# Optimization experiments

Measured on AMD Instinct MI355X. Metric: run time of the kernel, lower is better.

The kernel has to match this reference:

```python
import jax, jax.numpy as jnp
import numpy as np

NS_STEPS = 10
NS_A, NS_B, NS_C = 3.4445, -4.7750, 2.0315  # standard quintic Newton-Schulz coefficients
EPS = 1e-7

def orthogonalize(w):
    """Newton-Schulz iteration producing a (near-)orthogonal matrix from w."""
    din, dout = w.shape
    transpose = din > dout  # iterate on the wide orientation so X @ X.T is small
    x = w.T if transpose else w
    x = x / (jnp.linalg.norm(x) + EPS)  # spectral norm <= frobenius norm -> contraction

    def body(x, _):
        a = x @ x.T                      # (m, m) Gram matrix
        bmat = NS_B * a + NS_C * (a @ a)
        x = NS_A * x + bmat @ x
        return x, None

    x, _ = jax.lax.scan(body, x, None, length=NS_STEPS)
    return x.T if transpose else x


def setup_inputs() -> dict:
    key = jax.random.key(0)
    k1, k2, k3 = jax.random.split(key, 3)
    B, DIN, DOUT = 16384, 2048, 2048
    x = jax.random.normal(k1, (B, DIN), dtype=jnp.float32)
    w = jax.random.normal(k2, (DIN, DOUT), dtype=jnp.float32)
    b = jax.random.normal(k3, (DOUT,), dtype=jnp.float32) * 0.02
    return {"x": x, "w": w, "b": b}


def reference(x, w, b):
    w_orth = orthogonalize(w)
    return x @ w_orth + b
```

## Files before the change

kernel.cpp:

```cpp
#include <hip/hip_runtime.h>
#include <stdint.h>

typedef unsigned short u16;
typedef _Float16 half_t;
typedef __attribute__((ext_vector_type(4))) float f32x4;
typedef __attribute__((ext_vector_type(8))) _Float16 f16x8;

#define NS_A 3.4445f
#define NS_B -4.7750f
#define NS_C 2.0315f

#define SX      64.0f
#define INV_SX  (1.0f / 64.0f)
#define INV_SA  (1.0f / 4096.0f)

typedef const __attribute__((address_space(1))) void* as1_cvp;
typedef __attribute__((address_space(3))) void* as3_vp;
#define GLOAD_LDS16(gp, lp) \
    __builtin_amdgcn_global_load_lds((as1_cvp)(const void*)(gp), (as3_vp)(void*)(lp), 16, 0, 0)

template <int N> __device__ __forceinline__ void vmwait() {
    if constexpr (N == 0)       asm volatile("s_waitcnt vmcnt(0)" ::: "memory");
    else if constexpr (N == 4)  asm volatile("s_waitcnt vmcnt(4)" ::: "memory");
    else if constexpr (N == 6)  asm volatile("s_waitcnt vmcnt(6)" ::: "memory");
    else if constexpr (N == 8)  asm volatile("s_waitcnt vmcnt(8)" ::: "memory");
    else if constexpr (N == 12) asm volatile("s_waitcnt vmcnt(12)" ::: "memory");
    else static_assert(N == 0, "unsupported vmcnt");
}

template <int MODE>
__global__ __launch_bounds__(256, 2) void gemm_ns(
    const half_t* __restrict__ A, const half_t* __restrict__ B,
    const half_t* __restrict__ aux,
    void* __restrict__ outp, half_t* __restrict__ outpT,
    int M, int N, int K)
{
    __shared__ half_t As[3][64 * 64];
    __shared__ half_t Bs[3][128 * 64];
    const int tid  = threadIdx.x;
    const int wid  = tid >> 6;
    const int lane = tid & 63;
    const int wr = wid >> 1, wc = wid & 1;

    const int xcd = blockIdx.x & 7;
    const int ii  = blockIdx.x >> 3;
    const int brow = ((xcd & 1) * 16 + (ii >> 2)) * 64;
    const int bcol = ((xcd >> 1) * 4 + (ii & 3)) * 128;

    f32x4 acc[2][4] = {};

    const int r0   = tid >> 3;
    const int csrc = ((tid & 7) ^ ((tid >> 3) & 7)) * 8;
    const half_t* gA = A + (size_t)(brow + r0) * K + csrc;
    const half_t* gB = B + (size_t)(bcol + r0) * K + csrc;

    auto stage = [&](int slot, int kt) {
#pragma unroll
        for (int j = 0; j < 2; ++j)
            GLOAD_LDS16(gA + (size_t)(j * 32) * K + kt, &As[slot][(j * 256 + wid * 64) * 8]);
#pragma unroll
        for (int j = 0; j < 4; ++j)
            GLOAD_LDS16(gB + (size_t)(j * 32) * K + kt, &Bs[slot][(j * 256 + wid * 64) * 8]);
    };

    f16x8 af[2][2], bf[4][2];
    auto reads = [&](int slot) {
#pragma unroll
        for (int m = 0; m < 2; ++m) {
            const int row = wr * 32 + m * 16 + (lane & 15);
#pragma unroll
            for (int kk = 0; kk < 2; ++kk) {
                const int cc = (kk * 4 + (lane >> 4)) ^ (row & 7);
                af[m][kk] = *(const f16x8*)&As[slot][row * 64 + cc * 8];
            }
        }
#pragma unroll
        for (int n = 0; n < 4; ++n) {
            const int row = wc * 64 + n * 16 + (lane & 15);
#pragma unroll
            for (int kk = 0; kk < 2; ++kk) {
                const int cc = (kk * 4 + (lane >> 4)) ^ (row & 7);
                bf[n][kk] = *(const f16x8*)&Bs[slot][row * 64 + cc * 8];
            }
        }
    };
    auto mfma = [&]() {
        __builtin_amdgcn_s_setprio(1);
#pragma unroll
        for (int kk = 0; kk < 2; ++kk)
#pragma unroll
            for (int m = 0; m < 2; ++m)
#pragma unroll
                for (int n = 0; n < 4; ++n)
                    acc[m][n] = __builtin_amdgcn_mfma_f32_16x16x32_f16(af[m][kk], bf[n][kk], acc[m][n], 0, 0, 0);
        __builtin_amdgcn_s_setprio(0);
    };

    const int nsteps = K / 64;
    stage(0, 0);
    stage(1, 64);
    vmwait<6>();
    __builtin_amdgcn_s_barrier();

    int s = 0;
    for (; s < nsteps - 2; ++s) {
        reads(s % 3);
        stage((s + 2) % 3, (s + 2) * 64);
        vmwait<6>();
        __builtin_amdgcn_s_barrier();
        mfma();
        __builtin_amdgcn_s_barrier();
    }
    reads(s % 3);
    vmwait<0>();
    __builtin_amdgcn_s_barrier();
    mfma();
    __builtin_amdgcn_s_barrier();
    ++s;
    reads(s % 3);
    mfma();

#pragma unroll
    for (int m = 0; m < 2; ++m) {
#pragma unroll
        for (int n = 0; n < 4; ++n) {
            const int row0 = brow + wr * 32 + m * 16 + (lane >> 4) * 4;
            const int col  = bcol + wc * 64 + n * 16 + (lane & 15);
#pragma unroll
            for (int r = 0; r < 4; ++r) {
                const size_t idx = (size_t)(row0 + r) * N + col;
                const float v = acc[m][n][r];
                if (MODE == 0) {
                    ((half_t*)outp)[idx] = (half_t)v;
                } else if (MODE == 1) {
                    ((half_t*)outp)[idx] = (half_t)(NS_B * (float)aux[idx] + NS_C * v * INV_SA);
                } else {
                    const half_t o = (half_t)(NS_A * (float)aux[idx] + v * INV_SA);
                    ((half_t*)outp)[idx] = o;
                    if (outpT) outpT[(size_t)col * M + row0 + r] = o;
                }
            }
        }
    }
}

__global__ __launch_bounds__(512) void gemm_fin(
    const half_t* __restrict__ A, const half_t* __restrict__ B,
    const float* __restrict__ bias, float* __restrict__ out,
    int M, int N, int K)
{
    __shared__ half_t As[2][256 * 32];
    __shared__ half_t Bs[2][256 * 32];
    const int tid  = threadIdx.x;
    const int wid  = tid >> 6;
    const int lane = tid & 63;
    const int wm = wid >> 2;
    const int wn = wid & 3;

    int bid = blockIdx.x;
    const int cpx = gridDim.x >> 3;
    bid = (bid & 7) * cpx + (bid >> 3);
    const int nbx  = N >> 8;
    const int brow = (bid / nbx) << 8;
    const int bcol = (bid % nbx) << 8;

    f32x4 acc[8][4] = {};

    const int r0   = tid >> 2;
    const int csrc = ((tid & 3) ^ ((tid >> 3) & 3)) * 8;
    const half_t* gA = A + (size_t)(brow + r0) * K + csrc;
    const half_t* gB = B + (size_t)(bcol + r0) * K + csrc;

    auto stage = [&](int slot, int kt) {
#pragma unroll
        for (int j = 0; j < 2; ++j)
            GLOAD_LDS16(gA + (size_t)(j * 128) * K + kt, &As[slot][(j * 512 + wid * 64) * 8]);
#pragma unroll
        for (int j = 0; j < 2; ++j)
            GLOAD_LDS16(gB + (size_t)(j * 128) * K + kt, &Bs[slot][(j * 512 + wid * 64) * 8]);
    };
    auto compute = [&](int slot) {
        f16x8 af[8], bf[4];
#pragma unroll
        for (int fr = 0; fr < 8; ++fr) {
            const int row = wm * 128 + fr * 16 + (lane & 15);
            af[fr] = *(const f16x8*)&As[slot][row * 32 + (((lane >> 4) ^ ((row >> 1) & 3)) * 8)];
        }
#pragma unroll
        for (int fc = 0; fc < 4; ++fc) {
            const int row = wn * 64 + fc * 16 + (lane & 15);
            bf[fc] = *(const f16x8*)&Bs[slot][row * 32 + (((lane >> 4) ^ ((row >> 1) & 3)) * 8)];
        }
        __builtin_amdgcn_s_setprio(1);
#pragma unroll
        for (int fr = 0; fr < 8; ++fr)
#pragma unroll
            for (int fc = 0; fc < 4; ++fc)
                acc[fr][fc] = __builtin_amdgcn_mfma_f32_16x16x32_f16(af[fr], bf[fc], acc[fr][fc], 0, 0, 0);
        __builtin_amdgcn_s_setprio(0);
    };

    const int nsteps = K >> 5;
    stage(0, 0);
    vmwait<0>();
    __builtin_amdgcn_s_barrier();

    for (int s = 0; s < nsteps; ++s) {
        const int slot = s & 1;
        if (s + 1 < nsteps) stage(slot ^ 1, (s + 1) * 32);
        compute(slot);
        if (s + 1 < nsteps) {
            vmwait<0>();
            __builtin_amdgcn_s_barrier();
        }
    }

#pragma unroll
    for (int fr = 0; fr < 8; ++fr) {
#pragma unroll
        for (int fc = 0; fc < 4; ++fc) {
            const int row0 = brow + wm * 128 + fr * 16 + (lane >> 4) * 4;
            const int col  = bcol + wn * 64 + fc * 16 + (lane & 15);
            const float bv = bias[col];
#pragma unroll
            for (int r = 0; r < 4; ++r)
                out[(size_t)(row0 + r) * N + col] = acc[fr][fc][r] * INV_SX + bv;
        }
    }
}

__global__ __launch_bounds__(256) void k_sumsq(const float* __restrict__ w,
                                               float* __restrict__ part, int n) {
    __shared__ float s[256];
    const int per  = n / 1024;
    const int base = blockIdx.x * per;
    float acc = 0.f;
    for (int i = threadIdx.x; i < per; i += 256) {
        float v = w[base + i];
        acc += v * v;
    }
    s[threadIdx.x] = acc;
    __syncthreads();
    for (int k = 128; k > 0; k >>= 1) {
        if (threadIdx.x < k) s[threadIdx.x] += s[threadIdx.x + k];
        __syncthreads();
    }
    if (threadIdx.x == 0) part[blockIdx.x] = s[0];
}

__global__ __launch_bounds__(256) void k_scalefin(const float* __restrict__ part,
                                                  float* __restrict__ scale) {
    __shared__ float s[256];
    float acc = 0.f;
    for (int i = threadIdx.x; i < 1024; i += 256) acc += part[i];
    s[threadIdx.x] = acc;
    __syncthreads();
    for (int k = 128; k > 0; k >>= 1) {
        if (threadIdx.x < k) s[threadIdx.x] += s[threadIdx.x + k];
        __syncthreads();
    }
    if (threadIdx.x == 0) scale[0] = SX / (sqrtf(s[0]) + 1e-7f);
}

__global__ __launch_bounds__(256) void k_scale_f16(const float* __restrict__ w,
                                                   const float* __restrict__ scale,
                                                   half_t* __restrict__ o, int n) {
    const int i = (blockIdx.x * 256 + threadIdx.x) * 4;
    if (i < n) {
        const float sc = scale[0];
        float4 v = *(const float4*)(w + i);
        o[i + 0] = (half_t)(v.x * sc);
        o[i + 1] = (half_t)(v.y * sc);
        o[i + 2] = (half_t)(v.z * sc);
        o[i + 3] = (half_t)(v.w * sc);
    }
}

__global__ __launch_bounds__(256) void k_cast_f16(const float* __restrict__ w,
                                                  half_t* __restrict__ o, int n) {
    const int i = (blockIdx.x * 256 + threadIdx.x) * 4;
    if (i < n) {
        float4 v = *(const float4*)(w + i);
        o[i + 0] = (half_t)v.x;
        o[i + 1] = (half_t)v.y;
        o[i + 2] = (half_t)v.z;
        o[i + 3] = (half_t)v.w;
    }
}

__global__ __launch_bounds__(256) void k_transpose(const u16* __restrict__ in,
                                                   u16* __restrict__ out, int n) {
    __shared__ u16 tile[64][65];
    const int bx = blockIdx.x * 64, by = blockIdx.y * 64;
    const int tx = threadIdx.x & 63, ty = threadIdx.x >> 6;
    for (int i = ty; i < 64; i += 4) tile[i][tx] = in[(size_t)(by + i) * n + bx + tx];
    __syncthreads();
    for (int i = ty; i < 64; i += 4) out[(size_t)(bx + i) * n + by + tx] = tile[tx][i];
}

extern "C" void kernel_launch(void* const* d_in, const int* in_sizes, int n_in,
                              void* d_out, int out_size, void* d_ws, size_t ws_size,
                              hipStream_t stream) {
    const float* x = (const float*)d_in[0];
    const float* w = (const float*)d_in[1];
    const float* b = (const float*)d_in[2];
    float* out = (float*)d_out;

    const int D  = 2048;
    const int Bm = in_sizes[0] / D;
    const int WN = D * D;
    const int XN = Bm * D;

    const size_t matB = (size_t)WN * 2;
    const bool pingpong = ws_size >= 8192 + 6 * matB + (size_t)XN * 2;

    char* ws = (char*)d_ws;
    float* part  = (float*)ws;
    float* scale = part + 1024;
    half_t* xb0  = (half_t*)(ws + 8192);
    half_t* xb1  = xb0 + WN;
    half_t* xbTa = xb1 + WN;
    half_t* xbTb = pingpong ? (xbTa + WN) : xbTa;
    half_t* amat = xbTb + WN;
    half_t* bmat = amat + WN;
    half_t* xinb = bmat + WN;

    k_sumsq<<<1024, 256, 0, stream>>>(w, part, WN);
    k_scalefin<<<1, 256, 0, stream>>>(part, scale);
    k_scale_f16<<<WN / 4 / 256, 256, 0, stream>>>(w, scale, xb0, WN);

    k_cast_f16<<<XN / 4 / 256, 256, 0, stream>>>(x, xinb, XN);

    const dim3 tgrid(D / 64, D / 64);
    k_transpose<<<tgrid, 256, 0, stream>>>((const u16*)xb0, (u16*)xbTa, D);

    const int ns_grid = (D / 64) * (D / 128);

    half_t* cur = xb0;
    half_t* nxt = xb1;
    half_t* Tr  = xbTa;
    half_t* Tw  = xbTb;
    for (int it = 0; it < 10; ++it) {
        gemm_ns<0><<<ns_grid, 256, 0, stream>>>(cur, cur, nullptr, amat, nullptr, D, D, D);
        gemm_ns<1><<<ns_grid, 256, 0, stream>>>(amat, amat, amat, bmat, nullptr, D, D, D);
        if (pingpong) {
            gemm_ns<2><<<ns_grid, 256, 0, stream>>>(bmat, Tr, cur, nxt, Tw, D, D, D);
            half_t* tt = Tr; Tr = Tw; Tw = tt;
        } else {
            gemm_ns<2><<<ns_grid, 256, 0, stream>>>(bmat, Tr, cur, nxt, nullptr, D, D, D);
            k_transpose<<<tgrid, 256, 0, stream>>>((const u16*)nxt, (u16*)Tr, D);
        }
        half_t* t = cur; cur = nxt; nxt = t;
    }

    const int fin_grid = (Bm / 256) * (D / 256);
    gemm_fin<<<fin_grid, 512, 0, stream>>>(xinb, Tr, b, out, Bm, D, D);
}
```

Before: 964.4 us.

## Deepen final GEMM K-tile, fuse scale with transpose, skip unused last store

The final x@W GEMM now stages 64-wide K tiles instead of 32, with an 8-way XOR swizzle, so it needs half as many barrier/wait steps per block, at the cost of doubled LDS use. The scale-to-f16 kernel is merged with the initial transpose, which removes one launch and one pass over the weight matrix. The last Newton-Schulz iteration skips writing the row-major output, since only the transposed copy is consumed afterwards.

```diff
diff --git a/kernel.cpp b/kernel.cpp
--- a/kernel.cpp
+++ b/kernel.cpp
@@ -21,10 +21,7 @@
 
 template <int N> __device__ __forceinline__ void vmwait() {
     if constexpr (N == 0)       asm volatile("s_waitcnt vmcnt(0)" ::: "memory");
-    else if constexpr (N == 4)  asm volatile("s_waitcnt vmcnt(4)" ::: "memory");
     else if constexpr (N == 6)  asm volatile("s_waitcnt vmcnt(6)" ::: "memory");
-    else if constexpr (N == 8)  asm volatile("s_waitcnt vmcnt(8)" ::: "memory");
-    else if constexpr (N == 12) asm volatile("s_waitcnt vmcnt(12)" ::: "memory");
     else static_assert(N == 0, "unsupported vmcnt");
 }
 
@@ -136,7 +133,7 @@
                     ((half_t*)outp)[idx] = (half_t)(NS_B * (float)aux[idx] + NS_C * v * INV_SA);
                 } else {
                     const half_t o = (half_t)(NS_A * (float)aux[idx] + v * INV_SA);
-                    ((half_t*)outp)[idx] = o;
+                    if (outp)  ((half_t*)outp)[idx] = o;
                     if (outpT) outpT[(size_t)col * M + row0 + r] = o;
                 }
             }
@@ -149,8 +146,8 @@
     const float* __restrict__ bias, float* __restrict__ out,
     int M, int N, int K)
 {
-    __shared__ half_t As[2][256 * 32];
-    __shared__ half_t Bs[2][256 * 32];
+    __shared__ half_t As[2][256 * 64];
+    __shared__ half_t Bs[2][256 * 64];
     const int tid  = threadIdx.x;
     const int wid  = tid >> 6;
     const int lane = tid & 63;
@@ -166,48 +163,58 @@
 
     f32x4 acc[8][4] = {};
 
-    const int r0   = tid >> 2;
-    const int csrc = ((tid & 3) ^ ((tid >> 3) & 3)) * 8;
+    const int r0   = tid >> 3;
+    const int csrc = ((tid & 7) ^ ((tid >> 3) & 7)) * 8;
     const half_t* gA = A + (size_t)(brow + r0) * K + csrc;
     const half_t* gB = B + (size_t)(bcol + r0) * K + csrc;
 
     auto stage = [&](int slot, int kt) {
 #pragma unroll
-        for (int j = 0; j < 2; ++j)
-            GLOAD_LDS16(gA + (size_t)(j * 128) * K + kt, &As[slot][(j * 512 + wid * 64) * 8]);
-#pragma unroll
-        for (int j = 0; j < 2; ++j)
-            GLOAD_LDS16(gB + (size_t)(j * 128) * K + kt, &Bs[slot][(j * 512 + wid * 64) * 8]);
+        for (int j = 0; j < 4; ++j)
+            GLOAD_LDS16(gA + (size_t)(j * 64) * K + kt, &As[slot][(j * 512 + wid * 64) * 8]);
+#pragma unroll
+        for (int j = 0; j < 4; ++j)
+            GLOAD_LDS16(gB + (size_t)(j * 64) * K + kt, &Bs[slot][(j * 512 + wid * 64) * 8]);
     };
     auto compute = [&](int slot) {
-        f16x8 af[8], bf[4];
+        f16x8 af[8][2], bf[4][2];
 #pragma unroll
         for (int fr = 0; fr < 8; ++fr) {
             const int row = wm * 128 + fr * 16 + (lane & 15);
-            af[fr] = *(const f16x8*)&As[slot][row * 32 + (((lane >> 4) ^ ((row >> 1) & 3)) * 8)];
+#pragma unroll
+            for (int kk = 0; kk < 2; ++kk) {
+                const int cc = (kk * 4 + (lane >> 4)) ^ (row & 7);
+                af[fr][kk] = *(const f16x8*)&As[slot][row * 64 + cc * 8];
+            }
         }
 #pragma unroll
         for (int fc = 0; fc < 4; ++fc) {
             const int row = wn * 64 + fc * 16 + (lane & 15);
-            bf[fc] = *(const f16x8*)&Bs[slot][row * 32 + (((lane >> 4) ^ ((row >> 1) & 3)) * 8)];
+#pragma unroll
+            for (int kk = 0; kk < 2; ++kk) {
+                const int cc = (kk * 4 + (lane >> 4)) ^ (row & 7);
+                bf[fc][kk] = *(const f16x8*)&Bs[slot][row * 64 + cc * 8];
+            }
         }
         __builtin_amdgcn_s_setprio(1);
 #pragma unroll
-        for (int fr = 0; fr < 8; ++fr)
-#pragma unroll
-            for (int fc = 0; fc < 4; ++fc)
-                acc[fr][fc] = __builtin_amdgcn_mfma_f32_16x16x32_f16(af[fr], bf[fc], acc[fr][fc], 0, 0, 0);
+        for (int kk = 0; kk < 2; ++kk)
+#pragma unroll
+            for (int fr = 0; fr < 8; ++fr)
+#pragma unroll
+                for (int fc = 0; fc < 4; ++fc)
+                    acc[fr][fc] = __builtin_amdgcn_mfma_f32_16x16x32_f16(af[fr][kk], bf[fc][kk], acc[fr][fc], 0, 0, 0);
         __builtin_amdgcn_s_setprio(0);
     };
 
-    const int nsteps = K >> 5;
+    const int nsteps = K >> 6;
     stage(0, 0);
     vmwait<0>();
     __builtin_amdgcn_s_barrier();
 
     for (int s = 0; s < nsteps; ++s) {
         const int slot = s & 1;
-        if (s + 1 < nsteps) stage(slot ^ 1, (s + 1) * 32);
+        if (s + 1 < nsteps) stage(slot ^ 1, (s + 1) * 64);
         compute(slot);
         if (s + 1 < nsteps) {
             vmwait<0>();
@@ -262,18 +269,23 @@
     if (threadIdx.x == 0) scale[0] = SX / (sqrtf(s[0]) + 1e-7f);
 }
 
-__global__ __launch_bounds__(256) void k_scale_f16(const float* __restrict__ w,
-                                                   const float* __restrict__ scale,
-                                                   half_t* __restrict__ o, int n) {
-    const int i = (blockIdx.x * 256 + threadIdx.x) * 4;
-    if (i < n) {
-        const float sc = scale[0];
-        float4 v = *(const float4*)(w + i);
-        o[i + 0] = (half_t)(v.x * sc);
-        o[i + 1] = (half_t)(v.y * sc);
-        o[i + 2] = (half_t)(v.z * sc);
-        o[i + 3] = (half_t)(v.w * sc);
-    }
+__global__ __launch_bounds__(256) void k_scale_tr(const float* __restrict__ w,
+                                                  const float* __restrict__ scale,
+                                                  u16* __restrict__ o,
+                                                  u16* __restrict__ oT, int n) {
+    __shared__ u16 tile[64][65];
+    const int bx = blockIdx.x * 64, by = blockIdx.y * 64;
+    const int tx = threadIdx.x & 63, ty = threadIdx.x >> 6;
+    const float sc = scale[0];
+    for (int i = ty; i < 64; i += 4) {
+        const half_t h = (half_t)(w[(size_t)(by + i) * n + bx + tx] * sc);
+        const u16 u = __builtin_bit_cast(u16, h);
+        o[(size_t)(by + i) * n + bx + tx] = u;
+        tile[i][tx] = u;
+    }
+    __syncthreads();
+    for (int i = ty; i < 64; i += 4)
+        oT[(size_t)(bx + i) * n + by + tx] = tile[tx][i];
 }
 
 __global__ __launch_bounds__(256) void k_cast_f16(const float* __restrict__ w,
@@ -327,12 +339,10 @@
 
     k_sumsq<<<1024, 256, 0, stream>>>(w, part, WN);
     k_scalefin<<<1, 256, 0, stream>>>(part, scale);
-    k_scale_f16<<<WN / 4 / 256, 256, 0, stream>>>(w, scale, xb0, WN);
+    const dim3 tgrid(D / 64, D / 64);
+    k_scale_tr<<<tgrid, 256, 0, stream>>>(w, scale, (u16*)xb0, (u16*)xbTa, D);
 
     k_cast_f16<<<XN / 4 / 256, 256, 0, stream>>>(x, xinb, XN);
-
-    const dim3 tgrid(D / 64, D / 64);
-    k_transpose<<<tgrid, 256, 0, stream>>>((const u16*)xb0, (u16*)xbTa, D);
 
     const int ns_grid = (D / 64) * (D / 128);
 
@@ -344,7 +354,8 @@
         gemm_ns<0><<<ns_grid, 256, 0, stream>>>(cur, cur, nullptr, amat, nullptr, D, D, D);
         gemm_ns<1><<<ns_grid, 256, 0, stream>>>(amat, amat, amat, bmat, nullptr, D, D, D);
         if (pingpong) {
-            gemm_ns<2><<<ns_grid, 256, 0, stream>>>(bmat, Tr, cur, nxt, Tw, D, D, D);
+            half_t* outp = (it == 9) ? nullptr : nxt;
+            gemm_ns<2><<<ns_grid, 256, 0, stream>>>(bmat, Tr, cur, outp, Tw, D, D, D);
             half_t* tt = Tr; Tr = Tw; Tw = tt;
         } else {
             gemm_ns<2><<<ns_grid, 256, 0, stream>>>(bmat, Tr, cur, nxt, nullptr, D, D, D);
```

Result: faster. 943.4 us (median of 2 runs) (-2.2%).
